# Performance work log

Hardware: AMD Instinct MI355X
Metric: run time of the kernel (lower is better)

## Reference

```python
import jax, jax.numpy as jnp
import numpy as np

EPS = 1e-06

def rotate_half(x):
    d = x.shape[-1] // 2
    return jnp.concatenate([-x[..., d:], x[..., :d]], axis=-1)

def rmsnorm(x, w):
    rms = jnp.sqrt(jnp.mean(x * x, axis=-1, keepdims=True) + EPS)
    return (x / rms) * w

def setup_inputs() -> dict:
    key = jax.random.key(0)
    ks = jax.random.split(key, 12)
    H, Hq, Hkv, Dh, S, C = 2048, 16, 8, 128, 1, 16384
    sc = 0.02
    return {
        "hidden_states": jax.random.normal(ks[0], (1, 1, S, H), jnp.float32),
        "cos": jax.random.uniform(ks[1], (1, 1, S, Dh), jnp.float32),
        "sin": jax.random.uniform(ks[2], (1, 1, S, Dh), jnp.float32),
        "attention_mask": jnp.zeros((1, 1, S, C + S), jnp.float32),
        "k_cache": jax.random.normal(ks[3], (Hkv, Dh, C), jnp.float32),
        "v_cache": jax.random.normal(ks[4], (Hkv, C, Dh), jnp.float32),
        "Wq": jax.random.normal(ks[5], (Hq, Dh, H), jnp.float32) * sc,
        "Wk": jax.random.normal(ks[6], (Hkv, Dh, H), jnp.float32) * sc,
        "Wv": jax.random.normal(ks[7], (Hkv, Dh, H), jnp.float32) * sc,
        "Wo": jax.random.normal(ks[8], (H, Hq * Dh), jnp.float32) * sc,
        "q_norm_w": jnp.ones((Dh,), jnp.float32),
        "k_norm_w": jnp.ones((Dh,), jnp.float32),
    }

def reference(hidden_states, cos, sin, attention_mask, k_cache, v_cache, Wq, Wk, Wv, Wo, q_norm_w, k_norm_w):
    S = hidden_states.shape[2]
    Hq, Dh = Wq.shape[0], Wq.shape[1]
    Hkv = Wk.shape[0]
    g = Hq // Hkv
    x = hidden_states.reshape(S, -1)                      # [S, H]
    # per-head 1x1 conv == per-head linear; batched as einsum
    q = rmsnorm(jnp.einsum('sh,qdh->qsd', x, Wq), q_norm_w)   # [Hq, S, Dh]
    k = rmsnorm(jnp.einsum('sh,kdh->ksd', x, Wk), k_norm_w)   # [Hkv, S, Dh]
    v = jnp.einsum('sh,kdh->ksd', x, Wv)                      # [Hkv, S, Dh]
    c = cos.reshape(S, Dh)
    s = sin.reshape(S, Dh)
    q = q * c + rotate_half(q) * s
    k_new = k * c + rotate_half(k) * s
    # KV cache concat: k stored transposed [Hkv, Dh, C]
    k_full = jnp.concatenate([k_cache, jnp.swapaxes(k_new, 1, 2)], axis=2)  # [Hkv, Dh, C+S]
    v_full = jnp.concatenate([v_cache, v], axis=1)                          # [Hkv, C+S, Dh]
    kf = jnp.repeat(k_full, g, axis=0)                    # GQA expand -> [Hq, Dh, C+S]
    vf = jnp.repeat(v_full, g, axis=0)                    # [Hq, C+S, Dh]
    scaling = Dh ** -0.5
    scores = jnp.einsum('qsd,qdc->qsc', q, kf) * scaling + attention_mask.reshape(1, S, -1)
    probs = jax.nn.softmax(scores, axis=-1)
    out = jnp.einsum('qsc,qcd->qsd', probs, vf)           # [Hq, S, Dh]
    out = jnp.transpose(out, (1, 0, 2)).reshape(S, Hq * Dh)  # head-major last dim
    attn = out @ Wo.T                                     # o_proj 1x1 conv
    return attn.reshape(1, 1, S, -1), k_new, v
```

## Files before the change

### kernel.cpp

```cpp
#include <hip/hip_runtime.h>
#include <math.h>
#include <stddef.h>

#define HQ   16
#define HKV  8
#define DH   128
#define HID  2048
#define CC   16384
#define NCH  32
#define CHUNK 512


__global__ void k_qkv(const float* __restrict__ x,
                      const float* __restrict__ Wq,
                      const float* __restrict__ Wk,
                      const float* __restrict__ Wv,
                      float* __restrict__ raw,
                      float* __restrict__ out){
  int wave = threadIdx.x >> 6, lane = threadIdx.x & 63;
  int e = blockIdx.x * 4 + wave;
  const float* W;
  if (e < 2048)      W = Wq + (size_t)e * HID;
  else if (e < 3072) W = Wk + (size_t)(e - 2048) * HID;
  else               W = Wv + (size_t)(e - 3072) * HID;
  float4 wb[8], xb[8];
  #pragma unroll
  for (int j = 0; j < 8; ++j) wb[j] = *(const float4*)(W + (j * 64 + lane) * 4);
  #pragma unroll
  for (int j = 0; j < 8; ++j) xb[j] = *(const float4*)(x + (j * 64 + lane) * 4);
  __builtin_amdgcn_sched_barrier(0);
  float acc = 0.f;
  #pragma unroll
  for (int j = 0; j < 8; ++j)
    acc += wb[j].x*xb[j].x + wb[j].y*xb[j].y + wb[j].z*xb[j].z + wb[j].w*xb[j].w;
  #pragma unroll
  for (int off = 32; off; off >>= 1) acc += __shfl_down(acc, off, 64);
  if (lane == 0){
    raw[e] = acc;
    if (e >= 3072) out[e] = acc;
  }
}

__global__ void k_normrope(const float* __restrict__ raw,
                           const float* __restrict__ cosb,
                           const float* __restrict__ sinb,
                           const float* __restrict__ qw,
                           const float* __restrict__ kw,
                           float* __restrict__ qf,
                           float* __restrict__ kf,
                           float* __restrict__ out){
  __shared__ float lds[DH];
  __shared__ float wsum[2];
  int b = blockIdx.x, t = threadIdx.x;
  bool isq = (b < 16);
  int h = isq ? b : b - 16;
  float val = isq ? raw[h * DH + t] : raw[2048 + h * DH + t];
  float ss = val * val;
  #pragma unroll
  for (int off = 32; off; off >>= 1) ss += __shfl_down(ss, off, 64);
  if ((t & 63) == 0) wsum[t >> 6] = ss;
  __syncthreads();
  float rms = sqrtf((wsum[0] + wsum[1]) / 128.f + 1e-6f);
  float w = isq ? qw[t] : kw[t];
  float normed = val / rms * w;
  lds[t] = normed;
  __syncthreads();
  float rot = (t < 64) ? -lds[t + 64] : lds[t - 64];
  float res = normed * cosb[t] + rot * sinb[t];
  if (isq) qf[h * DH + t] = res;
  else { kf[h * DH + t] = res; out[2048 + h * DH + t] = res; }
}

__global__ __launch_bounds__(512) void k_flash(
    const float* __restrict__ qf,
    const float* __restrict__ kcache,
    const float* __restrict__ vcache,
    const float* __restrict__ mask,
    float* __restrict__ opart,
    float2* __restrict__ ml){
  __shared__ float q_s[2][DH];
  __shared__ float sc_part[8][2][CHUNK];
  __shared__ float p_s[2][CHUNK];
  __shared__ float part[2][16][DH];
  __shared__ float red[32];
  int kv = blockIdx.x >> 5, ch = blockIdx.x & 31;
  int c0 = ch << 9;
  int t = threadIdx.x;
  if (t < 256) q_s[t >> 7][t & 127] = qf[(kv * 2 + (t >> 7)) * DH + (t & 127)];
  __syncthreads();
  const float scale = 0.08838834764831845f;

  {
    int dg = t >> 6, ln = t & 63;
    const float* kp = kcache + (size_t)kv * DH * CC + (size_t)(dg * 16) * CC + c0 + ln * 4;
    float qr0[16], qr1[16];
    #pragma unroll
    for (int i = 0; i < 16; ++i){
      qr0[i] = q_s[0][dg * 16 + i];
      qr1[i] = q_s[1][dg * 16 + i];
    }
    #pragma unroll
    for (int half = 0; half < 2; ++half){
      const float* kph = kp + half * 256;
      float4 kb[8], kc2[8];
      #pragma unroll
      for (int j = 0; j < 8; ++j) kb[j]  = *(const float4*)(kph + (size_t)j * CC);
      #pragma unroll
      for (int j = 0; j < 8; ++j) kc2[j] = *(const float4*)(kph + (size_t)(j + 8) * CC);
      __builtin_amdgcn_sched_barrier(0);
      float a00 = 0.f, a01 = 0.f, a02 = 0.f, a03 = 0.f;
      float a10 = 0.f, a11 = 0.f, a12 = 0.f, a13 = 0.f;
      #pragma unroll
      for (int j = 0; j < 8; ++j){
        a00 += qr0[j] * kb[j].x;  a01 += qr0[j] * kb[j].y;
        a02 += qr0[j] * kb[j].z;  a03 += qr0[j] * kb[j].w;
        a10 += qr1[j] * kb[j].x;  a11 += qr1[j] * kb[j].y;
        a12 += qr1[j] * kb[j].z;  a13 += qr1[j] * kb[j].w;
      }
      #pragma unroll
      for (int j = 0; j < 8; ++j){
        a00 += qr0[8 + j] * kc2[j].x;  a01 += qr0[8 + j] * kc2[j].y;
        a02 += qr0[8 + j] * kc2[j].z;  a03 += qr0[8 + j] * kc2[j].w;
        a10 += qr1[8 + j] * kc2[j].x;  a11 += qr1[8 + j] * kc2[j].y;
        a12 += qr1[8 + j] * kc2[j].z;  a13 += qr1[8 + j] * kc2[j].w;
      }
      *(float4*)&sc_part[dg][0][half * 256 + ln * 4] = make_float4(a00, a01, a02, a03);
      *(float4*)&sc_part[dg][1][half * 256 + ln * 4] = make_float4(a10, a11, a12, a13);
    }
  }
  __syncthreads();

  int wv = t >> 6;
  float s0, s1;
  {
    float acc0 = 0.f, acc1 = 0.f;
    #pragma unroll
    for (int dg = 0; dg < 8; ++dg){
      acc0 += sc_part[dg][0][t];
      acc1 += sc_part[dg][1][t];
    }
    float mk = mask[c0 + t];
    s0 = acc0 * scale + mk;
    s1 = acc1 * scale + mk;
  }
  float lm0 = s0, lm1 = s1;
  #pragma unroll
  for (int off = 32; off; off >>= 1){
    lm0 = fmaxf(lm0, __shfl_down(lm0, off, 64));
    lm1 = fmaxf(lm1, __shfl_down(lm1, off, 64));
  }
  if ((t & 63) == 0){ red[wv] = lm0; red[8 + wv] = lm1; }
  __syncthreads();
  float m0 = red[0], m1 = red[8];
  #pragma unroll
  for (int i = 1; i < 8; ++i){
    m0 = fmaxf(m0, red[i]);
    m1 = fmaxf(m1, red[8 + i]);
  }
  float p0 = __expf(s0 - m0);
  float p1 = __expf(s1 - m1);
  p_s[0][t] = p0;
  p_s[1][t] = p1;
  float ls0 = p0, ls1 = p1;
  #pragma unroll
  for (int off = 32; off; off >>= 1){
    ls0 += __shfl_down(ls0, off, 64);
    ls1 += __shfl_down(ls1, off, 64);
  }
  if ((t & 63) == 0){ red[16 + wv] = ls0; red[24 + wv] = ls1; }
  __syncthreads();
  if (t == 0){
    float l0 = 0.f, l1 = 0.f;
    #pragma unroll
    for (int i = 0; i < 8; ++i){ l0 += red[16 + i]; l1 += red[24 + i]; }
    ml[(size_t)(kv * 2)     * NCH + ch] = make_float2(m0, l0);
    ml[(size_t)(kv * 2 + 1) * NCH + ch] = make_float2(m1, l1);
  }

  {
    int sl = t >> 5, d4 = (t & 31) * 4;
    const float* vbase = vcache + (size_t)kv * CC * DH + (size_t)c0 * DH + d4;
    float4 a0 = make_float4(0.f, 0.f, 0.f, 0.f);
    float4 a1 = make_float4(0.f, 0.f, 0.f, 0.f);
    #pragma unroll
    for (int ib = 0; ib < 4; ++ib){
      float4 vv[8];
      #pragma unroll
      for (int j = 0; j < 8; ++j){
        int off = (ib * 8 + j) * 16 + sl;
        vv[j] = *(const float4*)(vbase + (size_t)off * DH);
      }
      __builtin_amdgcn_sched_barrier(0);
      #pragma unroll
      for (int j = 0; j < 8; ++j){
        int off = (ib * 8 + j) * 16 + sl;
        float pp0 = p_s[0][off], pp1 = p_s[1][off];
        a0.x += pp0 * vv[j].x; a0.y += pp0 * vv[j].y; a0.z += pp0 * vv[j].z; a0.w += pp0 * vv[j].w;
        a1.x += pp1 * vv[j].x; a1.y += pp1 * vv[j].y; a1.z += pp1 * vv[j].z; a1.w += pp1 * vv[j].w;
      }
    }
    *(float4*)&part[0][sl][d4] = a0;
    *(float4*)&part[1][sl][d4] = a1;
  }
  __syncthreads();
  if (t < 256){
    int hh = t >> 7, d = t & 127;
    float o = 0.f;
    #pragma unroll
    for (int ss = 0; ss < 16; ++ss) o += part[hh][ss][d];
    int qh = kv * 2 + hh;
    opart[((size_t)qh * NCH + ch) * DH + d] = o;
  }
}

__global__ void k_combine(const float* __restrict__ opart,
                          const float2* __restrict__ ml,
                          const float* __restrict__ qf,
                          const float* __restrict__ kf,
                          const float* __restrict__ vnew,
                          const float* __restrict__ mask,
                          float* __restrict__ attn_in){
  __shared__ float osum[4][DH];
  __shared__ float Ls[4];
  __shared__ float redm[8];
  __shared__ float redq[2];
  int qh = blockIdx.x, t = threadIdx.x;
  int g = t >> 7, d = t & 127;
  int kv = qh >> 1;
  const float2* mlrow = ml + (size_t)qh * NCH;
  float mm = mlrow[t & 31].x;
  #pragma unroll
  for (int off = 32; off; off >>= 1) mm = fmaxf(mm, __shfl_down(mm, off, 64));
  if ((t & 63) == 0) redm[t >> 6] = mm;
  __syncthreads();
  float M = fmaxf(redm[0], redm[1]);
  float o = 0.f, L = 0.f;
  int ch0 = g * 8;
  #pragma unroll
  for (int i = 0; i < 8; ++i){
    float2 m2 = mlrow[ch0 + i];
    float w = __expf(m2.x - M);
    L += m2.y * w;
    o += w * opart[((size_t)qh * NCH + ch0 + i) * DH + d];
  }
  osum[g][d] = o;
  if (d == 0) Ls[g] = L;
  if (t < DH){
    float sum = qf[qh * DH + t] * kf[kv * DH + t];
    #pragma unroll
    for (int off = 32; off; off >>= 1) sum += __shfl_down(sum, off, 64);
    if ((t & 63) == 0) redq[t >> 6] = sum;
  }
  __syncthreads();
  if (t < DH){
    float s_new = (redq[0] + redq[1]) * 0.08838834764831845f + mask[CC];
    float pn = __expf(s_new - M);
    float Lf = Ls[0] + Ls[1] + Ls[2] + Ls[3] + pn;
    float of = osum[0][t] + osum[1][t] + osum[2][t] + osum[3][t]
             + pn * vnew[kv * DH + t];
    attn_in[qh * DH + t] = of / Lf;
  }
}

__global__ void k_oproj(const float* __restrict__ attn_in,
                        const float* __restrict__ Wo,
                        float* __restrict__ out){
  int wave = threadIdx.x >> 6, lane = threadIdx.x & 63;
  int e = blockIdx.x * 4 + wave;
  const float* W = Wo + (size_t)e * HID;
  float4 wb[8], xb[8];
  #pragma unroll
  for (int j = 0; j < 8; ++j) wb[j] = *(const float4*)(W + (j * 64 + lane) * 4);
  #pragma unroll
  for (int j = 0; j < 8; ++j) xb[j] = *(const float4*)(attn_in + (j * 64 + lane) * 4);
  __builtin_amdgcn_sched_barrier(0);
  float acc = 0.f;
  #pragma unroll
  for (int j = 0; j < 8; ++j)
    acc += wb[j].x*xb[j].x + wb[j].y*xb[j].y + wb[j].z*xb[j].z + wb[j].w*xb[j].w;
  #pragma unroll
  for (int off = 32; off; off >>= 1) acc += __shfl_down(acc, off, 64);
  if (lane == 0) out[e] = acc;
}

extern "C" void kernel_launch(void* const* d_in, const int* in_sizes, int n_in,
                              void* d_out, int out_size, void* d_ws, size_t ws_size,
                              hipStream_t stream){
  const float* x    = (const float*)d_in[0];
  const float* cosb = (const float*)d_in[1];
  const float* sinb = (const float*)d_in[2];
  const float* mask = (const float*)d_in[3];
  const float* kc   = (const float*)d_in[4];
  const float* vc   = (const float*)d_in[5];
  const float* Wq   = (const float*)d_in[6];
  const float* Wk   = (const float*)d_in[7];
  const float* Wv   = (const float*)d_in[8];
  const float* Wo   = (const float*)d_in[9];
  const float* qw   = (const float*)d_in[10];
  const float* kw   = (const float*)d_in[11];
  float* out = (float*)d_out;
  float* ws = (float*)d_ws;
  float* raw     = ws;
  float* qf      = ws + 4096;
  float* kf      = ws + 6144;
  float* opart   = ws + 8192;
  float2* ML     = (float2*)(ws + 73728);
  float* attn_in = ws + 74752;

  k_qkv     <<<1024, 256, 0, stream>>>(x, Wq, Wk, Wv, raw, out);
  k_normrope<<<24,   128, 0, stream>>>(raw, cosb, sinb, qw, kw, qf, kf, out);
  k_flash   <<<HKV * NCH, 512, 0, stream>>>(qf, kc, vc, mask, opart, ML);
  k_combine <<<HQ, 512, 0, stream>>>(opart, ML, qf, kf, raw + 3072, mask, attn_in);
  k_oproj   <<<512, 256, 0, stream>>>(attn_in, Wo, out);
}
```

Measured before the change: 212.9 us.

## Fuse norm/rope into flash and combine with o_proj into one kernel

Removes the separate norm+rope kernel by recomputing q normalization and RoPE inside each flash block. It also merges the split-softmax combine and the output projection into a single 32-block kernel that recomputes q/k norm, the new-token score and the combine redundantly per block before doing its slice of Wo. This cuts the launch count from five to three and drops intermediate buffers. In exchange, the Wo matrix-vector product runs on far fewer blocks, which may limit memory parallelism, and some work is duplicated across blocks.

```diff
diff --git a/kernel.cpp b/kernel.cpp
--- a/kernel.cpp
+++ b/kernel.cpp
@@ -41,38 +41,11 @@
   }
 }
 
-__global__ void k_normrope(const float* __restrict__ raw,
-                           const float* __restrict__ cosb,
-                           const float* __restrict__ sinb,
-                           const float* __restrict__ qw,
-                           const float* __restrict__ kw,
-                           float* __restrict__ qf,
-                           float* __restrict__ kf,
-                           float* __restrict__ out){
-  __shared__ float lds[DH];
-  __shared__ float wsum[2];
-  int b = blockIdx.x, t = threadIdx.x;
-  bool isq = (b < 16);
-  int h = isq ? b : b - 16;
-  float val = isq ? raw[h * DH + t] : raw[2048 + h * DH + t];
-  float ss = val * val;
-  #pragma unroll
-  for (int off = 32; off; off >>= 1) ss += __shfl_down(ss, off, 64);
-  if ((t & 63) == 0) wsum[t >> 6] = ss;
-  __syncthreads();
-  float rms = sqrtf((wsum[0] + wsum[1]) / 128.f + 1e-6f);
-  float w = isq ? qw[t] : kw[t];
-  float normed = val / rms * w;
-  lds[t] = normed;
-  __syncthreads();
-  float rot = (t < 64) ? -lds[t + 64] : lds[t - 64];
-  float res = normed * cosb[t] + rot * sinb[t];
-  if (isq) qf[h * DH + t] = res;
-  else { kf[h * DH + t] = res; out[2048 + h * DH + t] = res; }
-}
-
 __global__ __launch_bounds__(512) void k_flash(
-    const float* __restrict__ qf,
+    const float* __restrict__ raw,
+    const float* __restrict__ cosb,
+    const float* __restrict__ sinb,
+    const float* __restrict__ qw,
     const float* __restrict__ kcache,
     const float* __restrict__ vcache,
     const float* __restrict__ mask,
@@ -86,9 +59,25 @@
   int kv = blockIdx.x >> 5, ch = blockIdx.x & 31;
   int c0 = ch << 9;
   int t = threadIdx.x;
-  if (t < 256) q_s[t >> 7][t & 127] = qf[(kv * 2 + (t >> 7)) * DH + (t & 127)];
-  __syncthreads();
   const float scale = 0.08838834764831845f;
+
+  {
+    int w = t >> 6, l = t & 63;
+    if (w < 2){
+      int qh = kv * 2 + w;
+      const float* src = raw + qh * DH;
+      float v0 = src[l], v1 = src[l + 64];
+      float ss = v0 * v0 + v1 * v1;
+      #pragma unroll
+      for (int off = 32; off; off >>= 1) ss += __shfl_down(ss, off, 64);
+      ss = __shfl(ss, 0, 64);
+      float rms = sqrtf(ss * (1.f / 128.f) + 1e-6f);
+      float n0 = v0 / rms * qw[l], n1 = v1 / rms * qw[l + 64];
+      q_s[w][l]      = n0 * cosb[l]      - n1 * sinb[l];
+      q_s[w][l + 64] = n1 * cosb[l + 64] + n0 * sinb[l + 64];
+    }
+  }
+  __syncthreads();
 
   {
     int dg = t >> 6, ln = t & 63;
@@ -213,74 +202,104 @@
   }
 }
 
-__global__ void k_combine(const float* __restrict__ opart,
-                          const float2* __restrict__ ml,
-                          const float* __restrict__ qf,
-                          const float* __restrict__ kf,
-                          const float* __restrict__ vnew,
-                          const float* __restrict__ mask,
-                          float* __restrict__ attn_in){
-  __shared__ float osum[4][DH];
-  __shared__ float Ls[4];
-  __shared__ float redm[8];
-  __shared__ float redq[2];
-  int qh = blockIdx.x, t = threadIdx.x;
-  int g = t >> 7, d = t & 127;
-  int kv = qh >> 1;
-  const float2* mlrow = ml + (size_t)qh * NCH;
-  float mm = mlrow[t & 31].x;
-  #pragma unroll
-  for (int off = 32; off; off >>= 1) mm = fmaxf(mm, __shfl_down(mm, off, 64));
-  if ((t & 63) == 0) redm[t >> 6] = mm;
-  __syncthreads();
-  float M = fmaxf(redm[0], redm[1]);
-  float o = 0.f, L = 0.f;
-  int ch0 = g * 8;
-  #pragma unroll
-  for (int i = 0; i < 8; ++i){
-    float2 m2 = mlrow[ch0 + i];
-    float w = __expf(m2.x - M);
-    L += m2.y * w;
-    o += w * opart[((size_t)qh * NCH + ch0 + i) * DH + d];
-  }
-  osum[g][d] = o;
-  if (d == 0) Ls[g] = L;
-  if (t < DH){
-    float sum = qf[qh * DH + t] * kf[kv * DH + t];
-    #pragma unroll
-    for (int off = 32; off; off >>= 1) sum += __shfl_down(sum, off, 64);
-    if ((t & 63) == 0) redq[t >> 6] = sum;
-  }
-  __syncthreads();
-  if (t < DH){
-    float s_new = (redq[0] + redq[1]) * 0.08838834764831845f + mask[CC];
-    float pn = __expf(s_new - M);
-    float Lf = Ls[0] + Ls[1] + Ls[2] + Ls[3] + pn;
-    float of = osum[0][t] + osum[1][t] + osum[2][t] + osum[3][t]
-             + pn * vnew[kv * DH + t];
-    attn_in[qh * DH + t] = of / Lf;
-  }
-}
-
-__global__ void k_oproj(const float* __restrict__ attn_in,
-                        const float* __restrict__ Wo,
-                        float* __restrict__ out){
-  int wave = threadIdx.x >> 6, lane = threadIdx.x & 63;
-  int e = blockIdx.x * 4 + wave;
-  const float* W = Wo + (size_t)e * HID;
-  float4 wb[8], xb[8];
-  #pragma unroll
-  for (int j = 0; j < 8; ++j) wb[j] = *(const float4*)(W + (j * 64 + lane) * 4);
-  #pragma unroll
-  for (int j = 0; j < 8; ++j) xb[j] = *(const float4*)(attn_in + (j * 64 + lane) * 4);
-  __builtin_amdgcn_sched_barrier(0);
-  float acc = 0.f;
-  #pragma unroll
-  for (int j = 0; j < 8; ++j)
-    acc += wb[j].x*xb[j].x + wb[j].y*xb[j].y + wb[j].z*xb[j].z + wb[j].w*xb[j].w;
-  #pragma unroll
-  for (int off = 32; off; off >>= 1) acc += __shfl_down(acc, off, 64);
-  if (lane == 0) out[e] = acc;
+__global__ __launch_bounds__(512) void k_out(
+    const float* __restrict__ raw,
+    const float* __restrict__ cosb,
+    const float* __restrict__ sinb,
+    const float* __restrict__ qw,
+    const float* __restrict__ kw,
+    const float* __restrict__ opart,
+    const float2* __restrict__ ml,
+    const float* __restrict__ mask,
+    const float* __restrict__ Wo,
+    float* __restrict__ out){
+  __shared__ float qk_s[24][DH];
+  __shared__ float snew_s[HQ];
+  __shared__ float attn_s[HQ * DH];
+  int b = blockIdx.x, t = threadIdx.x;
+  int w = t >> 6, l = t & 63;
+  const float scale = 0.08838834764831845f;
+
+  #pragma unroll
+  for (int rep = 0; rep < 3; ++rep){
+    int r = w + rep * 8;
+    bool isq = (r < 16);
+    int h = isq ? r : r - 16;
+    const float* src = isq ? raw + h * DH : raw + 2048 + h * DH;
+    float v0 = src[l], v1 = src[l + 64];
+    float ss = v0 * v0 + v1 * v1;
+    #pragma unroll
+    for (int off = 32; off; off >>= 1) ss += __shfl_down(ss, off, 64);
+    ss = __shfl(ss, 0, 64);
+    float rms = sqrtf(ss * (1.f / 128.f) + 1e-6f);
+    const float* wt = isq ? qw : kw;
+    float n0 = v0 / rms * wt[l], n1 = v1 / rms * wt[l + 64];
+    qk_s[r][l]      = n0 * cosb[l]      - n1 * sinb[l];
+    qk_s[r][l + 64] = n1 * cosb[l + 64] + n0 * sinb[l + 64];
+  }
+  __syncthreads();
+
+  if (b == 0){
+    #pragma unroll
+    for (int rep = 0; rep < 2; ++rep){
+      int idx = t + rep * 512;
+      out[2048 + idx] = qk_s[16 + (idx >> 7)][idx & 127];
+    }
+  }
+
+  #pragma unroll
+  for (int rep = 0; rep < 2; ++rep){
+    int qh = w * 2 + rep;
+    int kvh = qh >> 1;
+    float p = qk_s[qh][l] * qk_s[16 + kvh][l]
+            + qk_s[qh][l + 64] * qk_s[16 + kvh][l + 64];
+    #pragma unroll
+    for (int off = 32; off; off >>= 1) p += __shfl_down(p, off, 64);
+    if (l == 0) snew_s[qh] = p * scale + mask[CC];
+  }
+  __syncthreads();
+
+  #pragma unroll
+  for (int rep = 0; rep < 4; ++rep){
+    int idx = t + rep * 512;
+    int qh = idx >> 7, d = idx & 127;
+    int kv = qh >> 1;
+    const float2* mlrow = ml + (size_t)qh * NCH;
+    float M = -1e30f;
+    #pragma unroll
+    for (int c = 0; c < NCH; ++c) M = fmaxf(M, mlrow[c].x);
+    float o = 0.f, L = 0.f;
+    #pragma unroll 4
+    for (int c = 0; c < NCH; ++c){
+      float2 m2 = mlrow[c];
+      float wgt = __expf(m2.x - M);
+      L += m2.y * wgt;
+      o += wgt * opart[((size_t)qh * NCH + c) * DH + d];
+    }
+    float pn = __expf(snew_s[qh] - M);
+    L += pn;
+    o += pn * raw[3072 + kv * DH + d];
+    attn_s[idx] = o / L;
+  }
+  __syncthreads();
+
+  #pragma unroll
+  for (int oo = 0; oo < 8; ++oo){
+    int e = b * 64 + w * 8 + oo;
+    const float* Wr = Wo + (size_t)e * HID;
+    float4 wb[8];
+    #pragma unroll
+    for (int j = 0; j < 8; ++j) wb[j] = *(const float4*)(Wr + (j * 64 + l) * 4);
+    float acc = 0.f;
+    #pragma unroll
+    for (int j = 0; j < 8; ++j){
+      float4 xf = *(const float4*)(attn_s + (j * 64 + l) * 4);
+      acc += wb[j].x*xf.x + wb[j].y*xf.y + wb[j].z*xf.z + wb[j].w*xf.w;
+    }
+    #pragma unroll
+    for (int off = 32; off; off >>= 1) acc += __shfl_down(acc, off, 64);
+    if (l == 0) out[e] = acc;
+  }
 }
 
 extern "C" void kernel_launch(void* const* d_in, const int* in_sizes, int n_in,
@@ -300,16 +319,13 @@
   const float* kw   = (const float*)d_in[11];
   float* out = (float*)d_out;
   float* ws = (float*)d_ws;
-  float* raw     = ws;
-  float* qf      = ws + 4096;
-  float* kf      = ws + 6144;
-  float* opart   = ws + 8192;
-  float2* ML     = (float2*)(ws + 73728);
-  float* attn_in = ws + 74752;
-
-  k_qkv     <<<1024, 256, 0, stream>>>(x, Wq, Wk, Wv, raw, out);
-  k_normrope<<<24,   128, 0, stream>>>(raw, cosb, sinb, qw, kw, qf, kf, out);
-  k_flash   <<<HKV * NCH, 512, 0, stream>>>(qf, kc, vc, mask, opart, ML);
-  k_combine <<<HQ, 512, 0, stream>>>(opart, ML, qf, kf, raw + 3072, mask, attn_in);
-  k_oproj   <<<512, 256, 0, stream>>>(attn_in, Wo, out);
+  float* raw   = ws;
+  float* opart = ws + 4096;
+  float2* ML   = (float2*)(ws + 69632);
+
+  k_qkv  <<<1024, 256, 0, stream>>>(x, Wq, Wk, Wv, raw, out);
+  k_flash<<<HKV * NCH, 512, 0, stream>>>(raw, cosb, sinb, qw, kc, vc, mask,
+                                         opart, ML);
+  k_out  <<<32, 512, 0, stream>>>(raw, cosb, sinb, qw, kw, opart, ML, mask,
+                                  Wo, out);
 }
```

After: 230.2 us. 8.2% more time.
